# Kernel tuning notes

Hardware: AMD Instinct MI355X
Metric: run time of the kernel (lower is better)

Reference implementation:

```python
import jax, jax.numpy as jnp
import numpy as np

B, C_IN, C_OUT, A, H, W = 32, 256, 512, 256, 64, 64


def setup_inputs() -> dict:
    key = jax.random.key(0)
    ks = jax.random.split(key, 8)
    s = 0.02
    return {
        "x": jax.random.normal(ks[0], (B, C_IN, H, W), dtype=jnp.float32),
        "g": jax.random.normal(ks[1], (B, C_OUT), dtype=jnp.float32),
        "Wg": jax.random.normal(ks[2], (A, C_OUT), dtype=jnp.float32) * s,
        "bg": jnp.full((A,), 0.1, dtype=jnp.float32),
        "Wx": jax.random.normal(ks[3], (A, C_IN), dtype=jnp.float32) * s,
        "bx": jnp.full((A,), 0.1, dtype=jnp.float32),
        "Wf": jax.random.normal(ks[4], (1, A), dtype=jnp.float32) * s,
        "bf": jnp.full((1,), 0.1, dtype=jnp.float32),
    }


def reference(x, g, Wg, bg, Wx, bx, Wf, bf):
    b, c, h, w = x.shape
    gg = g @ Wg.T + bg                                  # [B, A]
    xf = x.reshape(b, c, h * w)                          # [B, C, HW]
    # Linear_x applied per spatial position (batched instead of python loop)
    nx = jnp.einsum('bcn,ac->bna', xf, Wx) + bx          # [B, HW, A]
    nx = jax.nn.relu(gg[:, None, :] + nx)                # [B, HW, A]
    att = jnp.einsum('bna,a->bn', nx, Wf[0]) + bf[0]     # [B, HW]
    # min-subtract, sum-divide normalization
    att = att - jnp.min(att, axis=1, keepdims=True)
    att = att / jnp.sum(att, axis=1, keepdims=True)
    out = jnp.einsum('bcn,bn->bc', xf, att)              # weighted pooling [B, C]
    return out, att.reshape(b, h, w)
```

## Files before the change

### kernel.cpp

```cpp
#include <hip/hip_runtime.h>
#include <stdint.h>

#define B_   32
#define CIN  256
#define COUT 512
#define A_   256
#define HW_  4096
#define NT   64

typedef short  short8  __attribute__((ext_vector_type(8)));
typedef float  float4_ __attribute__((ext_vector_type(4)));

__device__ __forceinline__ unsigned short f2bf(float f) {
    unsigned u = __float_as_uint(f);
    u += 0x7FFFu + ((u >> 16) & 1u);
    return (unsigned short)(u >> 16);
}

__global__ __launch_bounds__(256) void prep_kernel(
    const float* __restrict__ g, const float* __restrict__ Wg,
    const float* __restrict__ bg, const float* __restrict__ Wx,
    const float* __restrict__ bx,
    unsigned short* __restrict__ Wxbf, float* __restrict__ ggbx,
    float* __restrict__ P, float* __restrict__ T)
{
    int b = blockIdx.x, t = threadIdx.x;
    int i = b * 256 + t;
    P[i] = 0.f; T[i] = 0.f;

    const float4* src = (const float4*)(Wx + (size_t)i * 8);
    float4 v0 = src[0], v1 = src[1];
    uint4 pk;
    pk.x = (unsigned)f2bf(v0.x) | ((unsigned)f2bf(v0.y) << 16);
    pk.y = (unsigned)f2bf(v0.z) | ((unsigned)f2bf(v0.w) << 16);
    pk.z = (unsigned)f2bf(v1.x) | ((unsigned)f2bf(v1.y) << 16);
    pk.w = (unsigned)f2bf(v1.z) | ((unsigned)f2bf(v1.w) << 16);
    *(uint4*)(Wxbf + (size_t)i * 8) = pk;

    __shared__ float gl[COUT];
    gl[t]       = g[b * COUT + t];
    gl[t + 256] = g[b * COUT + 256 + t];
    __syncthreads();

    float acc = bg[t] + bx[t];
    const float4* wr = (const float4*)(Wg + (size_t)t * COUT);
    #pragma unroll 4
    for (int co = 0; co < COUT / 4; co++) {
        float4 wv = wr[co];
        float4 gv = *(const float4*)&gl[co * 4];
        acc += wv.x * gv.x + wv.y * gv.y + wv.z * gv.z + wv.w * gv.w;
    }
    ggbx[b * 256 + t] = acc;
}

__global__ __launch_bounds__(256, 3) void attn_main(
    const float* __restrict__ x, const unsigned short* __restrict__ Wxbf,
    const float* __restrict__ ggbx, const float* __restrict__ Wf,
    const float* __restrict__ bfs,
    float* __restrict__ P, float* __restrict__ T, float* __restrict__ raw)
{
    __shared__ unsigned int xT[NT * 128];
    __shared__ float att_part[4][NT];
    __shared__ float raw_l[NT];

    int bid = blockIdx.x;
    int b = bid >> 6, nt = bid & 63;
    int t = threadIdx.x, w = t >> 6, lane = t & 63;
    int quad = lane >> 4, l15 = lane & 15;

    const float* xb = x + (size_t)b * CIN * HW_ + nt * NT;

    #pragma unroll
    for (int i = 0; i < 8; i++) {
        int c0 = 8 * (w + 4 * i);
        float v[8];
        #pragma unroll
        for (int j = 0; j < 8; j++) v[j] = xb[(size_t)(c0 + j) * HW_ + lane];
        uint4 pk;
        pk.x = (unsigned)f2bf(v[0]) | ((unsigned)f2bf(v[1]) << 16);
        pk.y = (unsigned)f2bf(v[2]) | ((unsigned)f2bf(v[3]) << 16);
        pk.z = (unsigned)f2bf(v[4]) | ((unsigned)f2bf(v[5]) << 16);
        pk.w = (unsigned)f2bf(v[6]) | ((unsigned)f2bf(v[7]) << 16);
        int q = c0 >> 3;
        *(uint4*)&xT[lane * 128 + ((q ^ (lane & 31)) << 2)] = pk;
    }

    float ga[4], wfv[4];
    #pragma unroll
    for (int ai = 0; ai < 4; ai++) {
        int a = w * 64 + ai * 16 + l15;
        ga[ai]  = ggbx[b * 256 + a];
        wfv[ai] = Wf[a];
    }
    __syncthreads();

    float4_ acc[4][4];
    #pragma unroll
    for (int mi = 0; mi < 4; mi++)
        #pragma unroll
        for (int ai = 0; ai < 4; ai++)
            acc[mi][ai] = (float4_){0.f, 0.f, 0.f, 0.f};

    for (int k0 = 0; k0 < CIN; k0 += 32) {
        int qk = (k0 >> 3) + quad;
        short8 af[4];
        #pragma unroll
        for (int mi = 0; mi < 4; mi++) {
            int n = mi * 16 + l15;
            af[mi] = *(const short8*)&xT[n * 128 + ((qk ^ (n & 31)) << 2)];
        }
        short8 bfr[4];
        #pragma unroll
        for (int ai = 0; ai < 4; ai++) {
            int a = w * 64 + ai * 16 + l15;
            bfr[ai] = *(const short8*)(Wxbf + (size_t)a * 256 + k0 + quad * 8);
        }
        #pragma unroll
        for (int mi = 0; mi < 4; mi++)
            #pragma unroll
            for (int ai = 0; ai < 4; ai++)
                acc[mi][ai] = __builtin_amdgcn_mfma_f32_16x16x32_bf16(
                    af[mi], bfr[ai], acc[mi][ai], 0, 0, 0);
    }

    #pragma unroll
    for (int mi = 0; mi < 4; mi++) {
        float p[4] = {0.f, 0.f, 0.f, 0.f};
        #pragma unroll
        for (int ai = 0; ai < 4; ai++) {
            #pragma unroll
            for (int r = 0; r < 4; r++) {
                float vv = acc[mi][ai][r] + ga[ai];
                vv = fmaxf(vv, 0.f);
                p[r] = fmaf(vv, wfv[ai], p[r]);
            }
        }
        #pragma unroll
        for (int r = 0; r < 4; r++) {
            #pragma unroll
            for (int off = 1; off < 16; off <<= 1)
                p[r] += __shfl_xor(p[r], off, 16);
        }
        if (l15 == 0) {
            #pragma unroll
            for (int r = 0; r < 4; r++)
                att_part[w][mi * 16 + quad * 4 + r] = p[r];
        }
    }
    __syncthreads();

    if (t < NT) {
        float rv = att_part[0][t] + att_part[1][t] + att_part[2][t] + att_part[3][t] + bfs[0];
        raw[b * HW_ + nt * NT + t] = rv;
        raw_l[t] = rv;
    }
    __syncthreads();

    float pp = 0.f, tt = 0.f;
    int q = t >> 3, dw = (t & 7) >> 1, hi = t & 1;
    #pragma unroll 8
    for (int n = 0; n < NT; n++) {
        unsigned u = xT[n * 128 + ((q ^ (n & 31)) << 2) + dw];
        unsigned short h = hi ? (unsigned short)(u >> 16) : (unsigned short)(u & 0xFFFFu);
        float xv = __uint_as_float(((unsigned)h) << 16);
        float rv = raw_l[n];
        pp = fmaf(xv, rv, pp);
        tt += xv;
    }
    atomicAdd(&P[b * 256 + t], pp);
    atomicAdd(&T[b * 256 + t], tt);
}

__global__ __launch_bounds__(256) void finalize_kernel(
    const float* __restrict__ raw, const float* __restrict__ P,
    const float* __restrict__ T, float* __restrict__ out)
{
    int b = blockIdx.x, t = threadIdx.x;
    const float* r = raw + (size_t)b * HW_;
    float v[16];
    float mn = 3.4e38f, sm = 0.f;
    #pragma unroll
    for (int i = 0; i < 16; i++) {
        v[i] = r[t + 256 * i];
        mn = fminf(mn, v[i]);
        sm += v[i];
    }
    #pragma unroll
    for (int off = 1; off < 64; off <<= 1) {
        mn = fminf(mn, __shfl_xor(mn, off, 64));
        sm += __shfl_xor(sm, off, 64);
    }
    __shared__ float smn[4], ssm[4];
    int w = t >> 6;
    if ((t & 63) == 0) { smn[w] = mn; ssm[w] = sm; }
    __syncthreads();
    mn = fminf(fminf(smn[0], smn[1]), fminf(smn[2], smn[3]));
    sm = (ssm[0] + ssm[1]) + (ssm[2] + ssm[3]);
    float S = sm - 4096.f * mn;
    float inv = 1.f / S;

    float* att = out + B_ * CIN + (size_t)b * HW_;
    #pragma unroll
    for (int i = 0; i < 16; i++) att[t + 256 * i] = (v[i] - mn) * inv;

    int ic = b * 256 + t;
    out[ic] = (P[ic] - mn * T[ic]) * inv;
}

extern "C" void kernel_launch(void* const* d_in, const int* in_sizes, int n_in,
                              void* d_out, int out_size, void* d_ws, size_t ws_size,
                              hipStream_t stream)
{
    const float* x   = (const float*)d_in[0];
    const float* g   = (const float*)d_in[1];
    const float* Wg  = (const float*)d_in[2];
    const float* bg  = (const float*)d_in[3];
    const float* Wx  = (const float*)d_in[4];
    const float* bx  = (const float*)d_in[5];
    const float* Wf  = (const float*)d_in[6];
    const float* bf  = (const float*)d_in[7];
    float* out = (float*)d_out;

    char* wsb = (char*)d_ws;
    unsigned short* Wxbf = (unsigned short*)wsb;
    float* ggbx = (float*)(wsb + 131072);
    float* P    = ggbx + 8192;
    float* T    = P + 8192;
    float* raw  = T + 8192;

    prep_kernel<<<32, 256, 0, stream>>>(g, Wg, bg, Wx, bx, Wxbf, ggbx, P, T);
    attn_main<<<2048, 256, 0, stream>>>(x, Wxbf, ggbx, Wf, bf, P, T, raw);
    finalize_kernel<<<32, 256, 0, stream>>>(raw, P, T, out);
}
```

Measured before the change: 261.9 us.

## Vectorize x tile loads, restructure pooling reduction, raise occupancy hint

The x tile load now uses float4 loads over four consecutive spatial positions per lane instead of scalar loads, reducing global load instruction count. The weighted-pooling stage has each thread read 4 channels over a 16-position slice via uint2 LDS reads, then reduces the per-wave partials through shared memory before the atomics. Launch bounds rise to 4 blocks per CU, and the small prep GEMV uses two accumulators. Risks are register pressure from 16 float4 registers under the tighter occupancy bound, and extra syncs.

```diff
diff --git a/kernel.cpp b/kernel.cpp
--- a/kernel.cpp
+++ b/kernel.cpp
@@ -11,10 +11,13 @@
 typedef short  short8  __attribute__((ext_vector_type(8)));
 typedef float  float4_ __attribute__((ext_vector_type(4)));
 
-__device__ __forceinline__ unsigned short f2bf(float f) {
+__device__ __forceinline__ unsigned f2bf(float f) {
     unsigned u = __float_as_uint(f);
     u += 0x7FFFu + ((u >> 16) & 1u);
-    return (unsigned short)(u >> 16);
+    return u >> 16;
+}
+__device__ __forceinline__ float bf2f(unsigned h) {
+    return __uint_as_float(h << 16);
 }
 
 __global__ __launch_bounds__(256) void prep_kernel(
@@ -31,10 +34,10 @@
     const float4* src = (const float4*)(Wx + (size_t)i * 8);
     float4 v0 = src[0], v1 = src[1];
     uint4 pk;
-    pk.x = (unsigned)f2bf(v0.x) | ((unsigned)f2bf(v0.y) << 16);
-    pk.y = (unsigned)f2bf(v0.z) | ((unsigned)f2bf(v0.w) << 16);
-    pk.z = (unsigned)f2bf(v1.x) | ((unsigned)f2bf(v1.y) << 16);
-    pk.w = (unsigned)f2bf(v1.z) | ((unsigned)f2bf(v1.w) << 16);
+    pk.x = f2bf(v0.x) | (f2bf(v0.y) << 16);
+    pk.y = f2bf(v0.z) | (f2bf(v0.w) << 16);
+    pk.z = f2bf(v1.x) | (f2bf(v1.y) << 16);
+    pk.w = f2bf(v1.z) | (f2bf(v1.w) << 16);
     *(uint4*)(Wxbf + (size_t)i * 8) = pk;
 
     __shared__ float gl[COUT];
@@ -42,18 +45,19 @@
     gl[t + 256] = g[b * COUT + 256 + t];
     __syncthreads();
 
-    float acc = bg[t] + bx[t];
+    float acc0 = bg[t] + bx[t], acc1 = 0.f;
     const float4* wr = (const float4*)(Wg + (size_t)t * COUT);
-    #pragma unroll 4
-    for (int co = 0; co < COUT / 4; co++) {
-        float4 wv = wr[co];
-        float4 gv = *(const float4*)&gl[co * 4];
-        acc += wv.x * gv.x + wv.y * gv.y + wv.z * gv.z + wv.w * gv.w;
-    }
-    ggbx[b * 256 + t] = acc;
-}
-
-__global__ __launch_bounds__(256, 3) void attn_main(
+    #pragma unroll 8
+    for (int co = 0; co < COUT / 4; co += 2) {
+        float4 wv0 = wr[co],     gv0 = *(const float4*)&gl[co * 4];
+        float4 wv1 = wr[co + 1], gv1 = *(const float4*)&gl[co * 4 + 4];
+        acc0 += wv0.x * gv0.x + wv0.y * gv0.y + wv0.z * gv0.z + wv0.w * gv0.w;
+        acc1 += wv1.x * gv1.x + wv1.y * gv1.y + wv1.z * gv1.z + wv1.w * gv1.w;
+    }
+    ggbx[b * 256 + t] = acc0 + acc1;
+}
+
+__global__ __launch_bounds__(256, 4) void attn_main(
     const float* __restrict__ x, const unsigned short* __restrict__ Wxbf,
     const float* __restrict__ ggbx, const float* __restrict__ Wf,
     const float* __restrict__ bfs,
@@ -70,19 +74,34 @@
 
     const float* xb = x + (size_t)b * CIN * HW_ + nt * NT;
 
-    #pragma unroll
-    for (int i = 0; i < 8; i++) {
-        int c0 = 8 * (w + 4 * i);
-        float v[8];
-        #pragma unroll
-        for (int j = 0; j < 8; j++) v[j] = xb[(size_t)(c0 + j) * HW_ + lane];
-        uint4 pk;
-        pk.x = (unsigned)f2bf(v[0]) | ((unsigned)f2bf(v[1]) << 16);
-        pk.y = (unsigned)f2bf(v[2]) | ((unsigned)f2bf(v[3]) << 16);
-        pk.z = (unsigned)f2bf(v[4]) | ((unsigned)f2bf(v[5]) << 16);
-        pk.w = (unsigned)f2bf(v[6]) | ((unsigned)f2bf(v[7]) << 16);
-        int q = c0 >> 3;
-        *(uint4*)&xT[lane * 128 + ((q ^ (lane & 31)) << 2)] = pk;
+    {
+        int sub = lane >> 4;
+        int n4  = (lane & 15) * 4;
+        int cb0 = w * 64 + sub * 8;
+        int cb1 = cb0 + 32;
+        float4_ v[16];
+        #pragma unroll
+        for (int j = 0; j < 8; j++)
+            v[j] = *(const float4_*)(xb + (size_t)(cb0 + j) * HW_ + n4);
+        #pragma unroll
+        for (int j = 0; j < 8; j++)
+            v[8 + j] = *(const float4_*)(xb + (size_t)(cb1 + j) * HW_ + n4);
+
+        #pragma unroll
+        for (int gq = 0; gq < 2; gq++) {
+            int q = (gq ? cb1 : cb0) >> 3;
+            const float4_* vg = &v[gq * 8];
+            #pragma unroll
+            for (int r = 0; r < 4; r++) {
+                uint4 pk;
+                pk.x = f2bf(vg[0][r]) | (f2bf(vg[1][r]) << 16);
+                pk.y = f2bf(vg[2][r]) | (f2bf(vg[3][r]) << 16);
+                pk.z = f2bf(vg[4][r]) | (f2bf(vg[5][r]) << 16);
+                pk.w = f2bf(vg[6][r]) | (f2bf(vg[7][r]) << 16);
+                int n = n4 + r;
+                *(uint4*)&xT[n * 128 + ((q ^ (n & 31)) << 2)] = pk;
+            }
+        }
     }
 
     float ga[4], wfv[4];
@@ -156,19 +175,38 @@
     }
     __syncthreads();
 
-    float pp = 0.f, tt = 0.f;
-    int q = t >> 3, dw = (t & 7) >> 1, hi = t & 1;
-    #pragma unroll 8
-    for (int n = 0; n < NT; n++) {
-        unsigned u = xT[n * 128 + ((q ^ (n & 31)) << 2) + dw];
-        unsigned short h = hi ? (unsigned short)(u >> 16) : (unsigned short)(u & 0xFFFFu);
-        float xv = __uint_as_float(((unsigned)h) << 16);
-        float rv = raw_l[n];
-        pp = fmaf(xv, rv, pp);
-        tt += xv;
-    }
-    atomicAdd(&P[b * 256 + t], pp);
-    atomicAdd(&T[b * 256 + t], tt);
+    float pp[4] = {0.f, 0.f, 0.f, 0.f};
+    float tt[4] = {0.f, 0.f, 0.f, 0.f};
+    {
+        int q    = (t & 63) >> 1;
+        int half = (t & 1) * 8;
+        int nb   = (t >> 6) * 16;
+        #pragma unroll
+        for (int i = 0; i < 16; i++) {
+            int n = nb + i;
+            uint2 u = *(const uint2*)((const char*)xT + n * 512 + ((q ^ (n & 31)) << 4) + half);
+            float rv = raw_l[n];
+            float x0 = bf2f(u.x & 0xFFFFu), x1 = bf2f(u.x >> 16);
+            float x2 = bf2f(u.y & 0xFFFFu), x3 = bf2f(u.y >> 16);
+            pp[0] = fmaf(x0, rv, pp[0]); tt[0] += x0;
+            pp[1] = fmaf(x1, rv, pp[1]); tt[1] += x1;
+            pp[2] = fmaf(x2, rv, pp[2]); tt[2] += x2;
+            pp[3] = fmaf(x3, rv, pp[3]); tt[3] += x3;
+        }
+    }
+    __syncthreads();
+    {
+        float* red = (float*)xT;
+        float4_* pr = (float4_*)(red + w * 512);
+        float4_* tr = (float4_*)(red + w * 512 + 256);
+        pr[t & 63] = (float4_){pp[0], pp[1], pp[2], pp[3]};
+        tr[t & 63] = (float4_){tt[0], tt[1], tt[2], tt[3]};
+        __syncthreads();
+        float Pc = red[t] + red[512 + t] + red[1024 + t] + red[1536 + t];
+        float Tc = red[256 + t] + red[768 + t] + red[1280 + t] + red[1792 + t];
+        atomicAdd(&P[b * 256 + t], Pc);
+        atomicAdd(&T[b * 256 + t], Tc);
+    }
 }
 
 __global__ __launch_bounds__(256) void finalize_kernel(
```

Result: faster. 251.5 us (-3.9%).
